# Kernel tuning notes

Measured on AMD Instinct MI355X. Metric: run time of the kernel, lower is better.

## Reference

```python
import jax, jax.numpy as jnp
import numpy as np

K = 16            # max_num_neighbors
RADIUS = 8.0      # interaction_radius
RBF = 128         # rbf_size == hidden_channels
HIDDEN = 128


def setup_inputs() -> dict:
    key = jax.random.key(0)
    k1, _ = jax.random.split(key)
    num_graphs = 64
    n_per_graph = 512
    # 3D coords; randn*3 gives realistic spread so radius mask is nontrivial
    pos = jax.random.normal(k1, (num_graphs * n_per_graph, 3), dtype=jnp.float32) * 3.0
    bias = jnp.zeros((HIDDEN,), dtype=jnp.float32)  # Parameter(zeros), requires_grad=False
    return {"pos": pos, "bias": bias, "num_graphs": num_graphs}


def reference(pos, bias, num_graphs):
    N = pos.shape[0]
    n = N // num_graphs                       # nodes per graph (uniform batch)
    p = pos.reshape(num_graphs, n, 3)
    # pairwise squared distances per graph: [B, n, n]
    d2 = jnp.sum((p[:, :, None, :] - p[:, None, :, :]) ** 2, axis=-1)
    # kNN with self-loop (loop=True): K+1 smallest distances per target node
    neg_d2, idx = jax.lax.top_k(-d2, K + 1)   # [B, n, K+1]
    d = jnp.sqrt(jnp.maximum(-neg_d2, 1e-12))
    # global edge_index: row = source (neighbor), col = target node
    graph_off = (jnp.arange(num_graphs) * n)[:, None, None]
    src = (idx + graph_off).reshape(-1)
    dst = jnp.broadcast_to(jnp.arange(n)[None, :, None] + graph_off,
                           (num_graphs, n, K + 1)).reshape(-1)
    edge_index = jnp.stack([src, dst])        # [2, B*n*(K+1)]
    dist = d.reshape(-1)
    # radius mask (original filters edges; we keep fixed shape and zero invalid rows)
    mask = dist <= RADIUS
    # Gaussian RBF distance embedding
    offsets = jnp.linspace(0.0, RADIUS, RBF, dtype=pos.dtype)
    coeff = -0.5 / (offsets[1] - offsets[0]) ** 2
    emb = jnp.exp(coeff * (dist[:, None] - offsets[None, :]) ** 2)  # [E, RBF]
    # forward: edge_repr = zeros + process_weight(dist); out = act(edge_repr + bias), act='none'
    edge_repr = emb + bias
    edge_repr = jnp.where(mask[:, None], edge_repr, 0.0)
    return edge_index, edge_repr, mask
```

## Files before the change

kernel.cpp:

```cpp
#include <hip/hip_runtime.h>
#include <math.h>

#define NPG   512
#define KK    17
#define RBFN  128
#define TPB   128
#define WPB   2
#define TPC   2
#define NSC   32
#define CPS   16
#define NCH   4
#define TGT_PER_WAVE (TPC * NCH)
#define TGT_PER_BLK  (WPB * TGT_PER_WAVE)
#define BPG   (NPG / TGT_PER_BLK)
#define LSTR  20

#define WAVE_SYNC()                                      \
  do {                                                   \
    asm volatile("s_waitcnt lgkmcnt(0)" ::: "memory");   \
    __builtin_amdgcn_sched_barrier(0);                   \
  } while (0)

__device__ __forceinline__ unsigned gmin32(unsigned v) {
  unsigned t;
  t = (unsigned)__builtin_amdgcn_ds_swizzle((int)v, 0x041F); v = v < t ? v : t;
  t = (unsigned)__builtin_amdgcn_ds_swizzle((int)v, 0x081F); v = v < t ? v : t;
  t = (unsigned)__builtin_amdgcn_ds_swizzle((int)v, 0x101F); v = v < t ? v : t;
  t = (unsigned)__builtin_amdgcn_ds_swizzle((int)v, 0x201F); v = v < t ? v : t;
  t = (unsigned)__builtin_amdgcn_ds_swizzle((int)v, 0x401F); v = v < t ? v : t;
  return v;
}

__global__ __launch_bounds__(TPB, 4) void fused_kernel(
    const float* __restrict__ pos, const float* __restrict__ bias,
    float* __restrict__ out, int E) {
  __shared__ float4 ps[NPG];
  __shared__ __align__(16) unsigned LA[WPB][64][LSTR];

  const int g = blockIdx.x / BPG;
  const int p = blockIdx.x % BPG;
  const float* gp = pos + (size_t)g * NPG * 3;
  for (int i = threadIdx.x; i < NPG; i += TPB)
    ps[i] = make_float4(gp[3 * i], gp[3 * i + 1], gp[3 * i + 2], 0.0f);
  __syncthreads();

  const int w = threadIdx.x >> 6;
  const int lane = threadIdx.x & 63;
  const int tl = lane >> 5;
  const int q = lane & 31;

  float* __restrict__ srcp = out;
  float* __restrict__ dstp = out + (size_t)E;
  float* __restrict__ repr = out + 2 * (size_t)E;
  float* __restrict__ mskp = out + 130 * (size_t)E;
  float4* __restrict__ repr4 = reinterpret_cast<float4*>(repr);

  const float step = 8.0f / 127.0f;
  const float coeff = -0.5f / (step * step);
  const int c0 = q << 2;
  const float4 bv = *reinterpret_cast<const float4*>(bias + c0);
  const float o0 = (float)(c0 + 0) * step, o1 = (float)(c0 + 1) * step,
              o2 = (float)(c0 + 2) * step, o3 = (float)(c0 + 3) * step;

  const int tbase = p * TGT_PER_BLK + w * TGT_PER_WAVE;
  const int goff = g * NPG;

  unsigned b0, b1, b2, b3, b4, b5, b6, b7, b8, b9, b10, b11, b12, b13, b14,
      b15;
  float px, py, pz;

#define CE(B)                                    \
  {                                              \
    const unsigned mn_ = key < (B) ? key : (B);  \
    const unsigned mx_ = key < (B) ? (B) : key;  \
    (B) = mn_;                                   \
    key = mx_;                                   \
  }

  for (int c = 0; c < NCH; ++c) {
    const int t = tbase + c * TPC + tl;
    {
      const float4 me = ps[t];
      px = me.x; py = me.y; pz = me.z;
    }
    b0 = b1 = b2 = b3 = b4 = b5 = b6 = b7 = b8 = b9 = b10 = b11 = b12 = b13 =
        b14 = b15 = 0xFFFFFFFFu;
#pragma unroll 4
    for (int jj = 0; jj < CPS; ++jj) {
      const int j = (jj << 5) | q;
      const float4 c4 = ps[j];
      const float dx = __fsub_rn(px, c4.x);
      const float dy = __fsub_rn(py, c4.y);
      const float dz = __fsub_rn(pz, c4.z);
      const float d2 = __fadd_rn(
          __fadd_rn(__fmul_rn(dx, dx), __fmul_rn(dy, dy)), __fmul_rn(dz, dz));
      unsigned key = (__float_as_uint(d2) & 0xFFFFFE00u) | (unsigned)j;
      CE(b0) CE(b1) CE(b2) CE(b3) CE(b4) CE(b5) CE(b6) CE(b7) CE(b8)
      CE(b9) CE(b10) CE(b11) CE(b12) CE(b13) CE(b14) CE(b15)
    }

    {
      uint4* Lv = reinterpret_cast<uint4*>(&LA[w][lane][0]);
      Lv[0] = make_uint4(b0, b1, b2, b3);
      Lv[1] = make_uint4(b4, b5, b6, b7);
      Lv[2] = make_uint4(b8, b9, b10, b11);
      Lv[3] = make_uint4(b12, b13, b14, b15);
      LA[w][lane][16] = 0xFFFFFFFFu;
    }
    WAVE_SYNC();

    const int node = goff + t;
    const size_t ebase = (size_t)node * KK;
    float4* __restrict__ rb = repr4 + (size_t)node * (KK * RBFN / 4);
    const unsigned* L = &LA[w][lane][0];
    int i = 0;
    unsigned h = L[0];
    unsigned cap = 0;
#pragma unroll
    for (int k = 0; k < KK; ++k) {
      const unsigned mn = gmin32(h);
      cap = (q == k) ? mn : cap;
      const int jv = (int)(mn & 511u);
      const float4 cj = ps[jv];
      const float dx = __fsub_rn(px, cj.x);
      const float dy = __fsub_rn(py, cj.y);
      const float dz = __fsub_rn(pz, cj.z);
      const float d2 = __fadd_rn(
          __fadd_rn(__fmul_rn(dx, dx), __fmul_rn(dy, dy)), __fmul_rn(dz, dz));
      const float dv = __fsqrt_rn(fmaxf(d2, 1e-12f));
      const float okf = (dv <= 8.0f) ? 1.0f : 0.0f;
      float4 o;
      { const float d_ = __fsub_rn(dv, o0); o.x = (__expf(coeff * d_ * d_) + bv.x) * okf; }
      { const float d_ = __fsub_rn(dv, o1); o.y = (__expf(coeff * d_ * d_) + bv.y) * okf; }
      { const float d_ = __fsub_rn(dv, o2); o.z = (__expf(coeff * d_ * d_) + bv.z) * okf; }
      { const float d_ = __fsub_rn(dv, o3); o.w = (__expf(coeff * d_ * d_) + bv.w) * okf; }
      rb[k * 32 + q] = o;
      const bool adv = (h == mn);
      i += adv;
      const unsigned nxt = L[i];
      h = adv ? nxt : h;
    }
    if (q < KK) {
      const int jv = (int)(cap & 511u);
      const float4 cj = ps[jv];
      const float dx = __fsub_rn(px, cj.x);
      const float dy = __fsub_rn(py, cj.y);
      const float dz = __fsub_rn(pz, cj.z);
      const float d2 = __fadd_rn(
          __fadd_rn(__fmul_rn(dx, dx), __fmul_rn(dy, dy)), __fmul_rn(dz, dz));
      const float dv = __fsqrt_rn(fmaxf(d2, 1e-12f));
      srcp[ebase + q] = (float)(jv + goff);
      dstp[ebase + q] = (float)node;
      mskp[ebase + q] = (dv <= 8.0f) ? 1.0f : 0.0f;
    }
    WAVE_SYNC();
  }
#undef CE
}

extern "C" void kernel_launch(void* const* d_in, const int* in_sizes, int n_in,
                              void* d_out, int out_size, void* d_ws, size_t ws_size,
                              hipStream_t stream) {
  const float* pos = (const float*)d_in[0];
  const float* bias = (const float*)d_in[1];
  (void)n_in; (void)d_ws; (void)ws_size; (void)out_size;

  const int N = in_sizes[0] / 3;
  const int B = N / NPG;
  const int E = N * KK;
  float* out = (float*)d_out;

  fused_kernel<<<B * BPG, TPB, 0, stream>>>(pos, bias, out, E);
}
```

Before: 56.69 us.

## Merge per-lane sorted lists in registers instead of LDS, halve targets per wave

The per-lane sorted candidate lists are no longer staged in LDS and walked with an index. The 17-step merge now pops the head by shifting all 16 register slots with selects. This removes the LDS scratch array, its stores and loads, and the wave syncs, so the occupancy hint rises from 4 to 8 blocks. Targets per wave drop from 4 to 2, which doubles the block count and repeats the shared-memory position load more often. The shift adds 16 v_cndmask per merge step.

```diff
diff --git a/kernel.cpp b/kernel.cpp
--- a/kernel.cpp
+++ b/kernel.cpp
@@ -9,17 +9,11 @@
 #define TPC   2
 #define NSC   32
 #define CPS   16
-#define NCH   4
+#define NCH   2
 #define TGT_PER_WAVE (TPC * NCH)
 #define TGT_PER_BLK  (WPB * TGT_PER_WAVE)
 #define BPG   (NPG / TGT_PER_BLK)
-#define LSTR  20
 
-#define WAVE_SYNC()                                      \
-  do {                                                   \
-    asm volatile("s_waitcnt lgkmcnt(0)" ::: "memory");   \
-    __builtin_amdgcn_sched_barrier(0);                   \
-  } while (0)
 
 __device__ __forceinline__ unsigned gmin32(unsigned v) {
   unsigned t;
@@ -31,11 +25,10 @@
   return v;
 }
 
-__global__ __launch_bounds__(TPB, 4) void fused_kernel(
+__global__ __launch_bounds__(TPB, 8) void fused_kernel(
     const float* __restrict__ pos, const float* __restrict__ bias,
     float* __restrict__ out, int E) {
   __shared__ float4 ps[NPG];
-  __shared__ __align__(16) unsigned LA[WPB][64][LSTR];
 
   const int g = blockIdx.x / BPG;
   const int p = blockIdx.x % BPG;
@@ -64,6 +57,7 @@
 
   const int tbase = p * TGT_PER_BLK + w * TGT_PER_WAVE;
   const int goff = g * NPG;
+  const unsigned SENT = 0xFFFFFFFFu;
 
   unsigned b0, b1, b2, b3, b4, b5, b6, b7, b8, b9, b10, b11, b12, b13, b14,
       b15;
@@ -84,7 +78,7 @@
       px = me.x; py = me.y; pz = me.z;
     }
     b0 = b1 = b2 = b3 = b4 = b5 = b6 = b7 = b8 = b9 = b10 = b11 = b12 = b13 =
-        b14 = b15 = 0xFFFFFFFFu;
+        b14 = b15 = SENT;
 #pragma unroll 4
     for (int jj = 0; jj < CPS; ++jj) {
       const int j = (jj << 5) | q;
@@ -99,26 +93,13 @@
       CE(b9) CE(b10) CE(b11) CE(b12) CE(b13) CE(b14) CE(b15)
     }
 
-    {
-      uint4* Lv = reinterpret_cast<uint4*>(&LA[w][lane][0]);
-      Lv[0] = make_uint4(b0, b1, b2, b3);
-      Lv[1] = make_uint4(b4, b5, b6, b7);
-      Lv[2] = make_uint4(b8, b9, b10, b11);
-      Lv[3] = make_uint4(b12, b13, b14, b15);
-      LA[w][lane][16] = 0xFFFFFFFFu;
-    }
-    WAVE_SYNC();
-
     const int node = goff + t;
     const size_t ebase = (size_t)node * KK;
     float4* __restrict__ rb = repr4 + (size_t)node * (KK * RBFN / 4);
-    const unsigned* L = &LA[w][lane][0];
-    int i = 0;
-    unsigned h = L[0];
     unsigned cap = 0;
 #pragma unroll
     for (int k = 0; k < KK; ++k) {
-      const unsigned mn = gmin32(h);
+      const unsigned mn = gmin32(b0);
       cap = (q == k) ? mn : cap;
       const int jv = (int)(mn & 511u);
       const float4 cj = ps[jv];
@@ -135,10 +116,15 @@
       { const float d_ = __fsub_rn(dv, o2); o.z = (__expf(coeff * d_ * d_) + bv.z) * okf; }
       { const float d_ = __fsub_rn(dv, o3); o.w = (__expf(coeff * d_ * d_) + bv.w) * okf; }
       rb[k * 32 + q] = o;
-      const bool adv = (h == mn);
-      i += adv;
-      const unsigned nxt = L[i];
-      h = adv ? nxt : h;
+      const bool adv = (b0 == mn);
+      b0  = adv ? b1  : b0;   b1  = adv ? b2  : b1;
+      b2  = adv ? b3  : b2;   b3  = adv ? b4  : b3;
+      b4  = adv ? b5  : b4;   b5  = adv ? b6  : b5;
+      b6  = adv ? b7  : b6;   b7  = adv ? b8  : b7;
+      b8  = adv ? b9  : b8;   b9  = adv ? b10 : b9;
+      b10 = adv ? b11 : b10;  b11 = adv ? b12 : b11;
+      b12 = adv ? b13 : b12;  b13 = adv ? b14 : b13;
+      b14 = adv ? b15 : b14;  b15 = adv ? SENT : b15;
     }
     if (q < KK) {
       const int jv = (int)(cap & 511u);
@@ -153,7 +139,6 @@
       dstp[ebase + q] = (float)node;
       mskp[ebase + q] = (dv <= 8.0f) ? 1.0f : 0.0f;
     }
-    WAVE_SYNC();
   }
 #undef CE
 }
```

New measurement: 52.01 us. -8.3%, faster.
